# Kernel tuning notes

Hardware: AMD Instinct MI355X
Metric: run time of the kernel (lower is better)

## Reference

```python
import jax, jax.numpy as jnp
import numpy as np

DN = ('NCHW', 'OIHW', 'NCHW')

def setup_inputs() -> dict:
    key = jax.random.key(0)
    ks = jax.random.split(key, 7)
    N, C_in, H, W = 32, 512, 56, 56
    C_sq, C_e1, C_e3 = 64, 256, 256
    def p(k, shape, fan_in):
        bound = 1.0 / np.sqrt(fan_in)
        return jax.random.uniform(k, shape, jnp.float32, -bound, bound)
    return {
        'x': jax.random.normal(ks[0], (N, C_in, H, W), jnp.float32),
        'w_sq': p(ks[1], (C_sq, C_in, 1, 1), C_in),
        'b_sq': p(ks[2], (C_sq,), C_in),
        'w_1x1': p(ks[3], (C_e1, C_sq, 1, 1), C_sq),
        'b_1x1': p(ks[4], (C_e1,), C_sq),
        'w_3x3': p(ks[5], (C_e3, C_sq, 3, 3), C_sq * 9),
        'b_3x3': p(ks[6], (C_e3,), C_sq * 9),
    }

def reference(x, w_sq, b_sq, w_1x1, b_1x1, w_3x3, b_3x3):
    # squeeze: 1x1 conv + ReLU
    s = jax.lax.conv_general_dilated(x, w_sq, (1, 1), 'VALID', dimension_numbers=DN)
    s = jax.nn.relu(s + b_sq[None, :, None, None])
    # expand 1x1 branch
    e1 = jax.lax.conv_general_dilated(s, w_1x1, (1, 1), 'VALID', dimension_numbers=DN)
    e1 = jax.nn.relu(e1 + b_1x1[None, :, None, None])
    # expand 3x3 branch, padding=1
    e3 = jax.lax.conv_general_dilated(s, w_3x3, (1, 1), ((1, 1), (1, 1)), dimension_numbers=DN)
    e3 = jax.nn.relu(e3 + b_3x3[None, :, None, None])
    return jnp.concatenate([e1, e3], axis=1)
```

## Files before the change

kernel.cpp:

```cpp
#include <hip/hip_runtime.h>
#include <hip/hip_bf16.h>
#include <stdint.h>

typedef __attribute__((ext_vector_type(8))) short bf16x8;
typedef __attribute__((ext_vector_type(4))) float f32x4;

#define GLB(p) ((const __attribute__((address_space(1))) void*)(p))
#define LDSP(p) ((__attribute__((address_space(3))) void*)(p))

#define HW    3136
#define WIMG  56
#define PROW  58
#define PNR   59
#define SIMG  (PNR * PROW)
#define C_IN  512

static __device__ __forceinline__ unsigned short f2bf(float f) {
    unsigned u = __builtin_bit_cast(unsigned, f);
    return (unsigned short)((u + 0x7FFFu + ((u >> 16) & 1u)) >> 16);
}

__global__ void prep_kernel(const float* __restrict__ wsq,
                            const float* __restrict__ w1,
                            const float* __restrict__ w3,
                            unsigned short* __restrict__ wsq_bf,
                            unsigned short* __restrict__ w1_bf,
                            unsigned short* __restrict__ w3r_bf,
                            unsigned short* __restrict__ s) {
    const int b = blockIdx.x, tid = threadIdx.x;
    if (b < 576) {
        int t = b * 256 + tid;
        if (t < 32768) wsq_bf[t] = f2bf(wsq[t]);
        if (t < 16384) w1_bf[t] = f2bf(w1[t]);
        int j = t >> 14, rem = t & 16383;
        int o = rem >> 6, c = rem & 63;
        w3r_bf[t] = f2bf(w3[(o * 64 + c) * 9 + j]);
    } else {
        const int img = b - 576;
        uint4* sn = (uint4*)(s + (size_t)img * SIMG * 64);
        uint4 z; z.x = z.y = z.z = z.w = 0;
        for (int t = tid; t < 1824; t += 256) {
            int cell = t >> 3, q = t & 7;
            int row, col;
            if (cell < 116) { row = (cell >= 58) ? 57 : 0; col = cell % 58; }
            else { int c2 = cell - 116; row = 1 + (c2 >> 1); col = (c2 & 1) * 57; }
            sn[(size_t)(row * PROW + col) * 8 + q] = z;
        }
    }
}

__global__ __launch_bounds__(256, 4) void squeeze_kernel(
    const float* __restrict__ x, const float* __restrict__ b_sq,
    const unsigned short* __restrict__ wsq_bf, unsigned short* __restrict__ s)
{
    const int n = blockIdx.y, hw0 = blockIdx.x * 64;
    const int tid = threadIdx.x;
    const int w = tid >> 6, l = tid & 63, lx = l & 15, lk = l >> 4;
    const int col = hw0 + w * 16 + lx;

    const float* xp = x + (size_t)n * C_IN * HW + col;
    const unsigned short* ap = wsq_bf + lx * C_IN + lk * 8;

    f32x4 acc[4] = {};
    for (int kb = 0; kb < 16; ++kb) {
        const int kbase = kb * 32 + lk * 8;
        float f[8];
        #pragma unroll
        for (int i = 0; i < 8; ++i) f[i] = xp[(size_t)(kbase + i) * HW];
        union { uint32_t u[4]; bf16x8 v; } bb;
        #pragma unroll
        for (int h = 0; h < 4; ++h)
            asm("v_cvt_pk_bf16_f32 %0, %1, %2" : "=v"(bb.u[h]) : "v"(f[2*h]), "v"(f[2*h+1]));
        bf16x8 a[4];
        #pragma unroll
        for (int mt = 0; mt < 4; ++mt)
            a[mt] = *(const bf16x8*)(ap + mt * 16 * C_IN + kb * 32);
        #pragma unroll
        for (int mt = 0; mt < 4; ++mt)
            acc[mt] = __builtin_amdgcn_mfma_f32_16x16x32_bf16(a[mt], bb.v, acc[mt], 0, 0, 0);
    }

    const int p = col + 59 + 2 * (col / WIMG);
    uint8_t* sn = (uint8_t*)s + (size_t)n * SIMG * 128 + (size_t)p * 128;
    const int psw = (p & 7) << 4;
    #pragma unroll
    for (int mt = 0; mt < 4; ++mt) {
        const int c0 = mt * 16 + lk * 4;
        float4 bias = *(const float4*)(b_sq + c0);
        const float* bp = (const float*)&bias;
        unsigned short v[4];
        #pragma unroll
        for (int r = 0; r < 4; ++r) v[r] = f2bf(fmaxf(acc[mt][r] + bp[r], 0.0f));
        uint2 pk;
        pk.x = (unsigned)v[0] | ((unsigned)v[1] << 16);
        pk.y = (unsigned)v[2] | ((unsigned)v[3] << 16);
        *(uint2*)(sn + ((c0 * 2) ^ psw)) = pk;
    }
}

__global__ __launch_bounds__(512, 2) void expand_kernel(
    const unsigned short* __restrict__ s,
    const unsigned short* __restrict__ w1_bf,
    const unsigned short* __restrict__ w3r_bf,
    const float* __restrict__ b1, const float* __restrict__ b3,
    float* __restrict__ out)
{
    __shared__ uint8_t tile[37120];
    const int bid = blockIdx.x;
    const int ord = (bid & 7) * 112 + (bid >> 3);
    const int n  = ord / 28;
    const int r2 = ord - n * 28;
    const int mt = r2 / 7;
    const int tg = r2 - mt * 7;

    const int tid = threadIdx.x;
    const int w = tid >> 6, l = tid & 63, lx = l & 15, lk = l >> 4;
    const int wm = w >> 1, wn = w & 1;
    const int cb = mt * 64 + wm * 16;
    const int lk16 = lk * 16;

    bf16x8 w1f[2], w3f[9][2];
    #pragma unroll
    for (int k0 = 0; k0 < 2; ++k0)
        w1f[k0] = *(const bf16x8*)(w1_bf + (cb + lx) * 64 + k0 * 32 + lk * 8);
    #pragma unroll
    for (int j = 0; j < 9; ++j)
        #pragma unroll
        for (int k0 = 0; k0 < 2; ++k0)
            w3f[j][k0] = *(const bf16x8*)(w3r_bf + j * 16384 + (cb + lx) * 64 + k0 * 32 + lk * 8);

    const float bias1 = b1[cb + lx];
    const float bias3 = b3[cb + lx];
    const uint8_t* sn = (const uint8_t*)s + (size_t)n * SIMG * 128;
    float* outn = out + (size_t)n * 512 * HW;

    uint4 g[5];
    {
        const int y0 = (tg * 7 * 64) / WIMG;
        const uint8_t* src = sn + (size_t)y0 * PROW * 128;
        #pragma unroll
        for (int it = 0; it < 4; ++it)
            g[it] = *(const uint4*)(src + (size_t)(it * 512 + tid) * 16);
        if (tid < 272) g[4] = *(const uint4*)(src + (size_t)(2048 + tid) * 16);
    }

    for (int t = 0; t < 7; ++t) {
        const int ht  = tg * 7 + t;
        const int hw0 = ht * 64;
        const int cy0 = hw0 / WIMG;

        __syncthreads();
        #pragma unroll
        for (int it = 0; it < 4; ++it)
            *(uint4*)&tile[(it * 512 + tid) * 16] = g[it];
        if (tid < 272) *(uint4*)&tile[(2048 + tid) * 16] = g[4];
        __syncthreads();

        if (t < 6) {
            const int ny0 = ((ht + 1) * 64) / WIMG;
            const uint8_t* src = sn + (size_t)ny0 * PROW * 128;
            #pragma unroll
            for (int it = 0; it < 4; ++it)
                g[it] = *(const uint4*)(src + (size_t)(it * 512 + tid) * 16);
            if (tid < 272) g[4] = *(const uint4*)(src + (size_t)(2048 + tid) * 16);
        }

        const int hb = hw0 + wn * 32;
        int pg[2], tb[2];
        #pragma unroll
        for (int nf = 0; nf < 2; ++nf) {
            int hw = hb + nf * 16 + lx;
            int p = hw + 59 + 2 * (hw / WIMG);
            pg[nf] = p;
            tb[nf] = (p - cy0 * PROW) * 128;
        }

        {
            f32x4 acc[2] = {};
            #pragma unroll
            for (int k0 = 0; k0 < 2; ++k0) {
                bf16x8 av[2];
                #pragma unroll
                for (int nf = 0; nf < 2; ++nf)
                    av[nf] = *(const bf16x8*)&tile[tb[nf] + ((lk16 + k0 * 64) ^ ((pg[nf] & 7) << 4))];
                #pragma unroll
                for (int nf = 0; nf < 2; ++nf)
                    acc[nf] = __builtin_amdgcn_mfma_f32_16x16x32_bf16(av[nf], w1f[k0], acc[nf], 0, 0, 0);
            }
            float* op = outn + (size_t)(cb + lx) * HW + hb + lk * 4;
            #pragma unroll
            for (int nf = 0; nf < 2; ++nf) {
                float4 v;
                v.x = fmaxf(acc[nf][0] + bias1, 0.0f);
                v.y = fmaxf(acc[nf][1] + bias1, 0.0f);
                v.z = fmaxf(acc[nf][2] + bias1, 0.0f);
                v.w = fmaxf(acc[nf][3] + bias1, 0.0f);
                *(float4*)(op + nf * 16) = v;
            }
        }

        {
            f32x4 acc[2] = {};
            #pragma unroll
            for (int j = 0; j < 9; ++j) {
                const int doff = (j / 3 - 1) * PROW + (j % 3 - 1);
                #pragma unroll
                for (int k0 = 0; k0 < 2; ++k0) {
                    bf16x8 av[2];
                    #pragma unroll
                    for (int nf = 0; nf < 2; ++nf) {
                        int pt = pg[nf] + doff;
                        av[nf] = *(const bf16x8*)&tile[tb[nf] + doff * 128 +
                                                      ((lk16 + k0 * 64) ^ ((pt & 7) << 4))];
                    }
                    #pragma unroll
                    for (int nf = 0; nf < 2; ++nf)
                        acc[nf] = __builtin_amdgcn_mfma_f32_16x16x32_bf16(av[nf], w3f[j][k0], acc[nf], 0, 0, 0);
                }
            }
            float* op = outn + (size_t)(256 + cb + lx) * HW + hb + lk * 4;
            #pragma unroll
            for (int nf = 0; nf < 2; ++nf) {
                float4 v;
                v.x = fmaxf(acc[nf][0] + bias3, 0.0f);
                v.y = fmaxf(acc[nf][1] + bias3, 0.0f);
                v.z = fmaxf(acc[nf][2] + bias3, 0.0f);
                v.w = fmaxf(acc[nf][3] + bias3, 0.0f);
                *(float4*)(op + nf * 16) = v;
            }
        }
    }
}

extern "C" void kernel_launch(void* const* d_in, const int* in_sizes, int n_in,
                              void* d_out, int out_size, void* d_ws, size_t ws_size,
                              hipStream_t stream) {
    const float* x   = (const float*)d_in[0];
    const float* wsq = (const float*)d_in[1];
    const float* bsq = (const float*)d_in[2];
    const float* w1  = (const float*)d_in[3];
    const float* b1  = (const float*)d_in[4];
    const float* w3  = (const float*)d_in[5];
    const float* b3  = (const float*)d_in[6];
    float* out = (float*)d_out;

    unsigned short* wsq_bf = (unsigned short*)d_ws;
    unsigned short* w1_bf  = wsq_bf + 32768;
    unsigned short* w3r_bf = w1_bf + 16384;
    unsigned short* s      = w3r_bf + 147456;

    prep_kernel<<<608, 256, 0, stream>>>(wsq, w1, w3, wsq_bf, w1_bf, w3r_bf, s);
    squeeze_kernel<<<dim3(49, 32), 256, 0, stream>>>(x, bsq, wsq_bf, s);
    expand_kernel<<<896, 512, 0, stream>>>(s, w1_bf, w3r_bf, b1, b3, out);
}
```

Baseline: 485.1 us.

## Stage squeeze input and expand tiles via double-buffered direct global-to-LDS loads

The squeeze kernel now stages 64-channel by 64-pixel slabs of x into a swizzled, double-buffered LDS region using global_load_lds. It then reads the operands from LDS instead of doing strided per-lane global loads, which is meant to improve coalescing and overlap loads with MFMA work. The expand kernel replaces its register-staged prefetch with asynchronous direct-to-LDS loads into two tile buffers and adds a barrier at the end of each iteration. Its launch bounds drop to one block per SIMD-group hint, which may relax register limits but doubles LDS use per block and can reduce occupancy.

New measurement: 420.7 us. -13.3%, faster.

```diff
diff --git a/kernel.cpp b/kernel.cpp
--- a/kernel.cpp
+++ b/kernel.cpp
@@ -53,33 +53,57 @@
     const float* __restrict__ x, const float* __restrict__ b_sq,
     const unsigned short* __restrict__ wsq_bf, unsigned short* __restrict__ s)
 {
+    __shared__ uint8_t xs[2][16384];
     const int n = blockIdx.y, hw0 = blockIdx.x * 64;
     const int tid = threadIdx.x;
     const int w = tid >> 6, l = tid & 63, lx = l & 15, lk = l >> 4;
+
+    const uint8_t* xbase = (const uint8_t*)(x + (size_t)n * C_IN * HW + hw0);
+
+    auto stage = [&](int buf, int kb) {
+        #pragma unroll
+        for (int q = 0; q < 4; ++q) {
+            int c = q * 256 + tid;
+            int r = c >> 4, g = c & 15;
+            const uint8_t* src = xbase + (size_t)(kb * 64 + r) * (HW * 4)
+                                       + ((g * 16) ^ (((r >> 3) & 3) << 6));
+            __builtin_amdgcn_global_load_lds(GLB(src), LDSP(&xs[buf][c * 16]), 16, 0, 0);
+        }
+    };
+
+    stage(0, 0);
+    __syncthreads();
+
+    f32x4 acc[4] = {};
+    const unsigned short* ap = wsq_bf + lx * C_IN + lk * 8;
+    const int colb4 = (w * 16 + lx) * 4;
+    const int swz = (lk & 3) << 6;
+
+    for (int kb = 0; kb < 8; ++kb) {
+        const int cur = kb & 1;
+        if (kb < 7) stage(cur ^ 1, kb + 1);
+        #pragma unroll
+        for (int kc = 0; kc < 2; ++kc) {
+            const uint8_t* bbase = &xs[cur][(kc * 32 + lk * 8) * 256 + (colb4 ^ swz)];
+            float f[8];
+            #pragma unroll
+            for (int i = 0; i < 8; ++i) f[i] = *(const float*)(bbase + i * 256);
+            union { uint32_t u[4]; bf16x8 v; } bb;
+            #pragma unroll
+            for (int h = 0; h < 4; ++h)
+                asm("v_cvt_pk_bf16_f32 %0, %1, %2" : "=v"(bb.u[h]) : "v"(f[2*h]), "v"(f[2*h+1]));
+            bf16x8 a[4];
+            #pragma unroll
+            for (int mt = 0; mt < 4; ++mt)
+                a[mt] = *(const bf16x8*)(ap + mt * 16 * C_IN + kb * 64 + kc * 32);
+            #pragma unroll
+            for (int mt = 0; mt < 4; ++mt)
+                acc[mt] = __builtin_amdgcn_mfma_f32_16x16x32_bf16(a[mt], bb.v, acc[mt], 0, 0, 0);
+        }
+        __syncthreads();
+    }
+
     const int col = hw0 + w * 16 + lx;
-
-    const float* xp = x + (size_t)n * C_IN * HW + col;
-    const unsigned short* ap = wsq_bf + lx * C_IN + lk * 8;
-
-    f32x4 acc[4] = {};
-    for (int kb = 0; kb < 16; ++kb) {
-        const int kbase = kb * 32 + lk * 8;
-        float f[8];
-        #pragma unroll
-        for (int i = 0; i < 8; ++i) f[i] = xp[(size_t)(kbase + i) * HW];
-        union { uint32_t u[4]; bf16x8 v; } bb;
-        #pragma unroll
-        for (int h = 0; h < 4; ++h)
-            asm("v_cvt_pk_bf16_f32 %0, %1, %2" : "=v"(bb.u[h]) : "v"(f[2*h]), "v"(f[2*h+1]));
-        bf16x8 a[4];
-        #pragma unroll
-        for (int mt = 0; mt < 4; ++mt)
-            a[mt] = *(const bf16x8*)(ap + mt * 16 * C_IN + kb * 32);
-        #pragma unroll
-        for (int mt = 0; mt < 4; ++mt)
-            acc[mt] = __builtin_amdgcn_mfma_f32_16x16x32_bf16(a[mt], bb.v, acc[mt], 0, 0, 0);
-    }
-
     const int p = col + 59 + 2 * (col / WIMG);
     uint8_t* sn = (uint8_t*)s + (size_t)n * SIMG * 128 + (size_t)p * 128;
     const int psw = (p & 7) << 4;
@@ -98,14 +122,14 @@
     }
 }
 
-__global__ __launch_bounds__(512, 2) void expand_kernel(
+__global__ __launch_bounds__(512, 1) void expand_kernel(
     const unsigned short* __restrict__ s,
     const unsigned short* __restrict__ w1_bf,
     const unsigned short* __restrict__ w3r_bf,
     const float* __restrict__ b1, const float* __restrict__ b3,
     float* __restrict__ out)
 {
-    __shared__ uint8_t tile[37120];
+    __shared__ uint8_t tile[2][37120];
     const int bid = blockIdx.x;
     const int ord = (bid & 7) * 112 + (bid >> 3);
     const int n  = ord / 28;
@@ -119,6 +143,21 @@
     const int cb = mt * 64 + wm * 16;
     const int lk16 = lk * 16;
 
+    const uint8_t* sn = (const uint8_t*)s + (size_t)n * SIMG * 128;
+    float* outn = out + (size_t)n * 512 * HW;
+
+    auto stage = [&](int buf, int ht) {
+        const int y0 = (ht * 64) / WIMG;
+        const uint8_t* src = sn + (size_t)y0 * PROW * 128;
+        #pragma unroll
+        for (int it = 0; it < 4; ++it)
+            __builtin_amdgcn_global_load_lds(GLB(src + (size_t)(it * 512 + tid) * 16),
+                                             LDSP(&tile[buf][(it * 512 + tid) * 16]), 16, 0, 0);
+        if (tid < 272)
+            __builtin_amdgcn_global_load_lds(GLB(src + (size_t)(2048 + tid) * 16),
+                                             LDSP(&tile[buf][(2048 + tid) * 16]), 16, 0, 0);
+    };
+
     bf16x8 w1f[2], w3f[9][2];
     #pragma unroll
     for (int k0 = 0; k0 < 2; ++k0)
@@ -128,42 +167,18 @@
         #pragma unroll
         for (int k0 = 0; k0 < 2; ++k0)
             w3f[j][k0] = *(const bf16x8*)(w3r_bf + j * 16384 + (cb + lx) * 64 + k0 * 32 + lk * 8);
-
     const float bias1 = b1[cb + lx];
     const float bias3 = b3[cb + lx];
-    const uint8_t* sn = (const uint8_t*)s + (size_t)n * SIMG * 128;
-    float* outn = out + (size_t)n * 512 * HW;
-
-    uint4 g[5];
-    {
-        const int y0 = (tg * 7 * 64) / WIMG;
-        const uint8_t* src = sn + (size_t)y0 * PROW * 128;
-        #pragma unroll
-        for (int it = 0; it < 4; ++it)
-            g[it] = *(const uint4*)(src + (size_t)(it * 512 + tid) * 16);
-        if (tid < 272) g[4] = *(const uint4*)(src + (size_t)(2048 + tid) * 16);
-    }
+
+    stage(0, tg * 7);
+    __syncthreads();
 
     for (int t = 0; t < 7; ++t) {
         const int ht  = tg * 7 + t;
         const int hw0 = ht * 64;
         const int cy0 = hw0 / WIMG;
-
-        __syncthreads();
-        #pragma unroll
-        for (int it = 0; it < 4; ++it)
-            *(uint4*)&tile[(it * 512 + tid) * 16] = g[it];
-        if (tid < 272) *(uint4*)&tile[(2048 + tid) * 16] = g[4];
-        __syncthreads();
-
-        if (t < 6) {
-            const int ny0 = ((ht + 1) * 64) / WIMG;
-            const uint8_t* src = sn + (size_t)ny0 * PROW * 128;
-            #pragma unroll
-            for (int it = 0; it < 4; ++it)
-                g[it] = *(const uint4*)(src + (size_t)(it * 512 + tid) * 16);
-            if (tid < 272) g[4] = *(const uint4*)(src + (size_t)(2048 + tid) * 16);
-        }
+        const int cur = t & 1;
+        if (t < 6) stage(cur ^ 1, ht + 1);
 
         const int hb = hw0 + wn * 32;
         int pg[2], tb[2];
@@ -174,6 +189,7 @@
             pg[nf] = p;
             tb[nf] = (p - cy0 * PROW) * 128;
         }
+        const uint8_t* tl = tile[cur];
 
         {
             f32x4 acc[2] = {};
@@ -182,7 +198,7 @@
                 bf16x8 av[2];
                 #pragma unroll
                 for (int nf = 0; nf < 2; ++nf)
-                    av[nf] = *(const bf16x8*)&tile[tb[nf] + ((lk16 + k0 * 64) ^ ((pg[nf] & 7) << 4))];
+                    av[nf] = *(const bf16x8*)&tl[tb[nf] + ((lk16 + k0 * 64) ^ ((pg[nf] & 7) << 4))];
                 #pragma unroll
                 for (int nf = 0; nf < 2; ++nf)
                     acc[nf] = __builtin_amdgcn_mfma_f32_16x16x32_bf16(av[nf], w1f[k0], acc[nf], 0, 0, 0);
@@ -210,8 +226,8 @@
                     #pragma unroll
                     for (int nf = 0; nf < 2; ++nf) {
                         int pt = pg[nf] + doff;
-                        av[nf] = *(const bf16x8*)&tile[tb[nf] + doff * 128 +
-                                                      ((lk16 + k0 * 64) ^ ((pt & 7) << 4))];
+                        av[nf] = *(const bf16x8*)&tl[tb[nf] + doff * 128 +
+                                                    ((lk16 + k0 * 64) ^ ((pt & 7) << 4))];
                     }
                     #pragma unroll
                     for (int nf = 0; nf < 2; ++nf)
@@ -229,6 +245,7 @@
                 *(float4*)(op + nf * 16) = v;
             }
         }
+        __syncthreads();
     }
 }
 
```
